# Performance work log

Hardware: AMD Instinct MI355X
Metric: run time of the kernel (lower is better)

## Reference

```python
import jax, jax.numpy as jnp
import numpy as np
import math

N, D, H, E = 4096, 128, 8, 131072
HD = D // H  # head_dim = 16
SCALE = 1.0 / math.sqrt(HD)


def ln(x, g, b, eps=1e-5):
    m = x.mean(-1, keepdims=True)
    v = ((x - m) ** 2).mean(-1, keepdims=True)
    return (x - m) * jax.lax.rsqrt(v + eps) * g + b


def setup_inputs() -> dict:
    key = jax.random.key(0)
    ks = iter(jax.random.split(key, 40))

    def lin(out_d, in_d):
        w = jax.random.normal(next(ks), (out_d, in_d), jnp.float32) / math.sqrt(in_d)
        b = jnp.zeros((out_d,), jnp.float32)
        return w, b

    x = jax.random.normal(next(ks), (N, D), jnp.float32)
    edge_index = jax.random.randint(next(ks), (2, E), 0, N, dtype=jnp.int64)
    wq_l, bq_l = lin(D, D); wk_l, bk_l = lin(D, D); wv_l, bv_l = lin(D, D)
    wg, bg = lin(D, 2 * D)
    wq_g, bq_g = lin(D, D); wk_g, bk_g = lin(D, D); wv_g, bv_g = lin(D, D)
    wo_g, bo_g = lin(D, D)
    wf, bf = lin(D, 2 * D)
    gf = jnp.ones((D,), jnp.float32); betaf = jnp.zeros((D,), jnp.float32)
    w1, b1 = lin(4 * D, D); w2, b2 = lin(D, 4 * D)
    g1 = jnp.ones((D,), jnp.float32); be1 = jnp.zeros((D,), jnp.float32)
    g2 = jnp.ones((D,), jnp.float32); be2 = jnp.zeros((D,), jnp.float32)
    return dict(x=x, edge_index=edge_index,
                wq_l=wq_l, bq_l=bq_l, wk_l=wk_l, bk_l=bk_l, wv_l=wv_l, bv_l=bv_l,
                wg=wg, bg=bg,
                wq_g=wq_g, bq_g=bq_g, wk_g=wk_g, bk_g=bk_g, wv_g=wv_g, bv_g=bv_g,
                wo_g=wo_g, bo_g=bo_g,
                wf=wf, bf=bf, gf=gf, betaf=betaf,
                w1=w1, b1=b1, w2=w2, b2=b2,
                g1=g1, be1=be1, g2=g2, be2=be2)


def reference(x, edge_index, wq_l, bq_l, wk_l, bk_l, wv_l, bv_l, wg, bg,
              wq_g, bq_g, wk_g, bk_g, wv_g, bv_g, wo_g, bo_g,
              wf, bf, gf, betaf, w1, b1, w2, b2, g1, be1, g2, be2):
    src, dst = edge_index[0], edge_index[1]  # PyG: j=source, i=target
    # ---- local edge-indexed multi-head attention (GraphInteractionModule) ----
    Q = (x @ wq_l.T + bq_l).reshape(N, H, HD)
    K = (x @ wk_l.T + bk_l).reshape(N, H, HD)
    V = (x @ wv_l.T + bv_l).reshape(N, H, HD)
    attn = (Q[dst] * K[src]).sum(-1) * SCALE            # [E, H]
    m = jax.ops.segment_max(attn, dst, num_segments=N)  # [N, H]
    e = jnp.exp(attn - m[dst])
    s = jax.ops.segment_sum(e, dst, num_segments=N)
    alpha = e / s[dst]                                  # segment softmax over edges into each dst
    agg = jax.ops.segment_sum(V[src] * alpha[..., None], dst, num_segments=N).reshape(N, D)
    gate = jax.nn.sigmoid(jnp.concatenate([x, agg], axis=-1) @ wg.T + bg)
    local = gate * agg + (1.0 - gate) * x
    # ---- global dense MHA over all nodes (B=1) ----
    xn = ln(x, g1, be1)
    q = (xn @ wq_g.T + bq_g).reshape(N, H, HD)
    k = (xn @ wk_g.T + bk_g).reshape(N, H, HD)
    v = (xn @ wv_g.T + bv_g).reshape(N, H, HD)
    scores = jnp.einsum('nhd,mhd->hnm', q, k) * SCALE   # [H, N, N]
    p = jax.nn.softmax(scores, axis=-1)
    go = jnp.einsum('hnm,mhd->nhd', p, v).reshape(N, D) @ wo_g.T + bo_g
    # ---- fusion + residual + FFN ----
    fused = jax.nn.relu(ln(jnp.concatenate([local, go], axis=-1) @ wf.T + bf, gf, betaf))
    h = x + fused
    h2 = ln(h, g2, be2)
    out = h + (jax.nn.gelu(h2 @ w1.T + b1, approximate=False) @ w2.T + b2)
    return out
```

## Files before the change

kernel.cpp:

```cpp
#include <hip/hip_runtime.h>
#include <math.h>

#define NN 4096
#define DM 128
#define NE 131072
#define QSCALE 0.36067376022224085f
#define ESCALE 0.36067376022224085f

typedef short short8 __attribute__((ext_vector_type(8)));
typedef float f32x4  __attribute__((ext_vector_type(4)));
typedef unsigned int uint4v __attribute__((ext_vector_type(4)));

static __device__ __forceinline__ unsigned pk2(float lo, float hi) {
  union { float f; unsigned u; } a, b; a.f = lo; b.f = hi;
  return __builtin_amdgcn_perm(b.u + 0x8000u, a.u + 0x8000u, 0x07060302u);
}
static __device__ __forceinline__ unsigned pkp(float lo, float hi) {
  union { float f; unsigned u; } a, b; a.f = lo; b.f = hi;
  return __builtin_amdgcn_perm(b.u, a.u, 0x07060302u);
}
static __device__ __forceinline__ unsigned short f2bh(float f) {
  union { float f; unsigned u; } v; v.f = f;
  return (unsigned short)((v.u + 0x8000u) >> 16);
}
// ... 70 lines not shown
  }
  const int g = blockIdx.y >> 1;
  const float* Wt  = (g==0)?W0:(g==1)?W1:(g==2)?W2:(g==3)?W3:(g==4)?W4:W5;
  const float* Bia = (g==0)?B0:(g==1)?B1:(g==2)?B2:(g==3)?B3:(g==4)?B4:B5;
  void* Cp         = (g==0)?O0:(g==1)?O1:(g==2)?O2:(g==3)?O3:(g==4)?O4:O5;
  const int omode  = (g==4)?3:(g==5)?2:1;
  const float osc  = (g==3)? QSCALE : (g==0)? ESCALE : 1.f;
  const int m0 = blockIdx.x * 64, n0 = (blockIdx.y & 1) * 64;
  const int tid = threadIdx.x;
  const int srow = tid >> 2, koff = (tid & 3) * 8;
  const int lane = tid & 63, wave = tid >> 6;
  const int quad = lane >> 4, m16 = lane & 15;

  const float* arow = X + (size_t)(m0 + srow) * 128 + koff;
  float4 a0[4], a1[4];
#pragma unroll
  for (int c = 0; c < 4; c++) {
    a0[c] = *(const float4*)(arow + c * 32);
    a1[c] = *(const float4*)(arow + c * 32 + 4);
  }
  if (g >= 3) {
    float s = 0.f;
#pragma unroll
    for (int c = 0; c < 4; c++)
      s += a0[c].x + a0[c].y + a0[c].z + a0[c].w + a1[c].x + a1[c].y + a1[c].z + a1[c].w;
    s += __shfl_xor(s, 1); s += __shfl_xor(s, 2);
    float mean = s * (1.0f / 128.0f);
    float v = 0.f;
#pragma unroll
    for (int c = 0; c < 4; c++) {
      float d;
      d = a0[c].x - mean; v += d*d;  d = a0[c].y - mean; v += d*d;
      d = a0[c].z - mean; v += d*d;  d = a0[c].w - mean; v += d*d;
      d = a1[c].x - mean; v += d*d;  d = a1[c].y - mean; v += d*d;
      d = a1[c].z - mean; v += d*d;  d = a1[c].w - mean; v += d*d;
    }
    v += __shfl_xor(v, 1); v += __shfl_xor(v, 2);
    float rstd = rsqrtf(v * (1.0f / 128.0f) + 1e-5f);
#pragma unroll
    for (int c = 0; c < 4; c++) {
      const int col = c * 32 + koff;
      float4 gv0 = *(const float4*)(G1 + col),  gv1 = *(const float4*)(G1 + col + 4);
      float4 bv0 = *(const float4*)(Be1 + col), bv1 = *(const float4*)(Be1 + col + 4);
      LN1(a0[c].x, gv0.x, bv0.x); LN1(a0[c].y, gv0.y, bv0.y);
      LN1(a0[c].z, gv0.z, bv0.z); LN1(a0[c].w, gv0.w, bv0.w);
      LN1(a1[c].x, gv1.x, bv1.x); LN1(a1[c].y, gv1.y, bv1.y);
      LN1(a1[c].z, gv1.z, bv1.z); LN1(a1[c].w, gv1.w, bv1.w);
    }
  }

  f32x4 acc[4];
#pragma unroll
  for (int i = 0; i < 4; i++) acc[i] = {0.f, 0.f, 0.f, 0.f};
#pragma unroll
  for (int c = 0; c < 4; c++) {
    const float* wp = Wt + (size_t)(n0 + srow) * 128 + c * 32 + koff;
    float4 w0 = *(const float4*)wp, w1v = *(const float4*)(wp + 4);
    __syncthreads();
    *(short8*)&Asm[srow][koff] = cvt8(a0[c], a1[c]);
    *(short8*)&Wsm[srow][koff] = cvt8(w0, w1v);
    __syncthreads();
    short8 af = *(short8*)&Asm[wave * 16 + m16][quad * 8];
#pragma unroll
    for (int nt = 0; nt < 4; nt++) {
      short8 bf = *(short8*)&Wsm[nt * 16 + m16][quad * 8];
      acc[nt] = __builtin_amdgcn_mfma_f32_16x16x32_bf16(af, bf, acc[nt], 0, 0, 0);
    }
  }
#pragma unroll
  for (int nt = 0; nt < 4; nt++) {
#pragma unroll
    for (int r = 0; r < 4; r++) {
      const int m = m0 + wave * 16 + quad * 4 + r;
      const int n = n0 + nt * 16 + m16;
      float v = (acc[nt][r] + Bia[n]) * osc;
      size_t oi = (size_t)m * 128 + n;
      if (omode == 1)      ((unsigned short*)Cp)[oi] = f2bh(v);
      else if (omode == 3) ((unsigned short*)Cp)[(size_t)(n >> 4) * (NN * 16) + (size_t)m * 16 + (n & 15)] = f2bh(v);
      else                 ((unsigned short*)Cp)[(size_t)n * NN + m] = f2bh(v);
    }
  }
}

__global__ __launch_bounds__(256) void gemm_gate(
    const float* __restrict__ X, const float* __restrict__ AGG,
    const float* __restrict__ Wg, const float* __restrict__ Bg,
    float* __restrict__ LOCAL)
{
  __shared__ short Asm[64][40];
  __shared__ short Wsm[64][40];
  const int m0 = blockIdx.x * 64, n0 = blockIdx.y * 64;
  const int tid = threadIdx.x;
  const int srow = tid >> 2, koff = (tid & 3) * 8;
  const int lane = tid & 63, wave = tid >> 6;
  const int quad = lane >> 4, m16 = lane & 15;
  f32x4 acc[4];
#pragma unroll
  for (int i = 0; i < 4; i++) acc[i] = {0.f, 0.f, 0.f, 0.f};

  for (int k0 = 0; k0 < 256; k0 += 32) {
    const int kg = k0 + koff;
    const float* ap = (kg < 128) ? (X + (size_t)(m0 + srow) * 128 + kg)
                                 : (AGG + (size_t)(m0 + srow) * 128 + (kg - 128));
    float4 a0 = *(const float4*)ap, a1 = *(const float4*)(ap + 4);
    const float* wp = Wg + (size_t)(n0 + srow) * 256 + kg;
    float4 w0 = *(const float4*)wp, w1v = *(const float4*)(wp + 4);
    __syncthreads();
    *(short8*)&Asm[srow][koff] = cvt8(a0, a1);
    *(short8*)&Wsm[srow][koff] = cvt8(w0, w1v);
    __syncthreads();
    short8 af = *(short8*)&Asm[wave * 16 + m16][quad * 8];
#pragma unroll
    for (int nt = 0; nt < 4; nt++) {
      short8 bf = *(short8*)&Wsm[nt * 16 + m16][quad * 8];
      acc[nt] = __builtin_amdgcn_mfma_f32_16x16x32_bf16(af, bf, acc[nt], 0, 0, 0);
    }
  }
#pragma unroll
  for (int nt = 0; nt < 4; nt++) {
#pragma unroll
    for (int r = 0; r < 4; r++) {
      const int m = m0 + wave * 16 + quad * 4 + r;
      const int n = n0 + nt * 16 + m16;
      float v = acc[nt][r] + Bg[n];
      size_t oi = (size_t)m * 128 + n;
      float gg = 1.0f / (1.0f + __expf(fminf(fmaxf(-v, -80.f), 80.f)));
      LOCAL[oi] = gg * AGG[oi] + (1.0f - gg) * X[oi];
    }
  }
}

__global__ __launch_bounds__(256) void gemm_fuse(
    const float* __restrict__ LOCAL, const float* __restrict__ GO,
    const float* __restrict__ WF, const float* __restrict__ WC,
    const float* __restrict__ BF, const float* __restrict__ BFOLD,
    float* __restrict__ OUT)
{
  __shared__ short Asm[64][40];
  __shared__ short Wsm[64][40];
  const int m0 = blockIdx.x * 64, n0 = blockIdx.y * 64;
  const int tid = threadIdx.x;
  const int srow = tid >> 2, koff = (tid & 3) * 8;
  const int lane = tid & 63, wave = tid >> 6;
  const int quad = lane >> 4, m16 = lane & 15;
  f32x4 acc[4];
#pragma unroll
  for (int i = 0; i < 4; i++) acc[i] = {0.f, 0.f, 0.f, 0.f};

  for (int k0 = 0; k0 < 256; k0 += 32) {
    const int kg = k0 + koff;
    const float* ap = (kg < 128) ? (LOCAL + (size_t)(m0 + srow) * 128 + kg)
                                 : (GO + (size_t)(m0 + srow) * 128 + (kg - 128));
    float4 a0 = *(const float4*)ap, a1 = *(const float4*)(ap + 4);
    const float* wp = (kg < 128) ? (WF + (size_t)(n0 + srow) * 256 + kg)
                                 : (WC + (size_t)(n0 + srow) * 128 + (kg - 128));
    float4 w0 = *(const float4*)wp, w1v = *(const float4*)(wp + 4);
    __syncthreads();
    *(short8*)&Asm[srow][koff] = cvt8(a0, a1);
    *(short8*)&Wsm[srow][koff] = cvt8(w0, w1v);
    __syncthreads();
    short8 af = *(short8*)&Asm[wave * 16 + m16][quad * 8];
#pragma unroll
    for (int nt = 0; nt < 4; nt++) {
      short8 bf = *(short8*)&Wsm[nt * 16 + m16][quad * 8];
      acc[nt] = __builtin_amdgcn_mfma_f32_16x16x32_bf16(af, bf, acc[nt], 0, 0, 0);
    }
  }
#pragma unroll
  for (int nt = 0; nt < 4; nt++) {
#pragma unroll
    for (int r = 0; r < 4; r++) {
      const int m = m0 + wave * 16 + quad * 4 + r;
      const int n = n0 + nt * 16 + m16;
      size_t oi = (size_t)m * 128 + n;
      OUT[oi] = acc[nt][r] + BF[n] + BFOLD[n];
    }
  }
}

__global__ __launch_bounds__(512) void k_attn_fused(
    const unsigned short* __restrict__ Kh, const unsigned short* __restrict__ Qb,
    const unsigned short* __restrict__ VT, float* __restrict__ O,
    const int* __restrict__ EI, const unsigned short* __restrict__ Qb16,
    const unsigned short* __restrict__ Kb16,
    unsigned short* __restrict__ EB, int* __restrict__ deg)
{
  __shared__ float LO[8][4][16][16];
  __shared__ float LL[8][4][16];
  if (blockIdx.x >= 512) {
    int is64 = detect64(EI);
    int gid = (blockIdx.x - 512) * 512 + threadIdx.x;
    int e = gid >> 3, hh = gid & 7;
    int s = is64 ? EI[2*e]      : EI[e];
    int d = is64 ? EI[2*(NE+e)] : EI[NE+e];
    s = min(max(s, 0), NN-1); d = min(max(d, 0), NN-1);
    const uint4v* qp = (const uint4v*)(Qb16 + (size_t)d * DM + hh * 16);
    const uint4v* kp = (const uint4v*)(Kb16 + (size_t)s * DM + hh * 16);
    uint4v qa = qp[0], qb2 = qp[1];
    uint4v ka = kp[0], kb2 = kp[1];
    float acc = 0.f;
#pragma unroll
    for (int i2 = 0; i2 < 4; i2++) {
      acc += blo(qa[i2]) * blo(ka[i2]) + bhi(qa[i2]) * bhi(ka[i2]);
      acc += blo(qb2[i2]) * blo(kb2[i2]) + bhi(qb2[i2]) * bhi(kb2[i2]);
    }
    EB[(size_t)e*8 + hh] = f2bh(__builtin_amdgcn_exp2f(fminf(acc, 43.0f)));
    if (hh == 0) atomicAdd(&deg[d], 1);
    return;
  }
  const int h = blockIdx.x >> 6, qt = blockIdx.x & 63;
  const int tid = threadIdx.x, lane = tid & 63, wave = tid >> 6;
  const int quad = lane >> 4, m16 = lane & 15;
  const int r0 = qt * 64;
  const short8 z8 = {0,0,0,0,0,0,0,0};
  const f32x4  z4 = {0.f,0.f,0.f,0.f};
  short8 qf[4] = {z8, z8, z8, z8};
  if (quad < 2) {
#pragma unroll
    for (int j = 0; j < 4; j++)
      qf[j] = *(const short8*)(Qb + (size_t)(r0 + j * 16 + m16) * DM + h * 16 + quad * 8);
  }
  short8 ones;
#pragma unroll
  for (int i = 0; i < 8; i++) ones[i] = (short)0x3F80;
  const int kperm = (m16 >> 2) * 8 + (m16 & 3);
  const int kbase = wave * 512;
  const unsigned short* khead = Kh + (size_t)h * (NN * 16);
  f32x4 acc[4] = {z4, z4, z4, z4};
  f32x4 acc2[4] = {z4, z4, z4, z4};
  short8 a0 = z8, a1 = z8, a2 = z8, a3 = z8;
  for (int kt = 0; kt < 8; kt++) {
    const int key0 = kbase + kt * 64;
    if (quad < 2) {
      const unsigned short* kp = khead + (size_t)(key0 + kperm) * 16 + quad * 8;
      a0 = *(const short8*)kp;
      a1 = *(const short8*)(kp + 4 * 16);
      a2 = *(const short8*)(kp + 32 * 16);
      a3 = *(const short8*)(kp + 36 * 16);
    }
    const unsigned short* vp = VT + (size_t)(h * 16 + m16) * NN + key0 + quad * 8;
    short8 av0 = *(const short8*)vp;
    short8 av1 = *(const short8*)(vp + 32);
#pragma unroll
    for (int j = 0; j < 4; j++) {
      f32x4 s0 = __builtin_amdgcn_mfma_f32_16x16x32_bf16(a0, qf[j], z4, 0, 0, 0);
      f32x4 s1 = __builtin_amdgcn_mfma_f32_16x16x32_bf16(a1, qf[j], z4, 0, 0, 0);
      f32x4 s2 = __builtin_amdgcn_mfma_f32_16x16x32_bf16(a2, qf[j], z4, 0, 0, 0);
      f32x4 s3 = __builtin_amdgcn_mfma_f32_16x16x32_bf16(a3, qf[j], z4, 0, 0, 0);
      float e0 = __builtin_amdgcn_exp2f(s0[0]), e1 = __builtin_amdgcn_exp2f(s0[1]);
      float e2 = __builtin_amdgcn_exp2f(s0[2]), e3 = __builtin_amdgcn_exp2f(s0[3]);
      float e4 = __builtin_amdgcn_exp2f(s1[0]), e5 = __builtin_amdgcn_exp2f(s1[1]);
      float e6 = __builtin_amdgcn_exp2f(s1[2]), e7 = __builtin_amdgcn_exp2f(s1[3]);
      uint4v u;
      u.x = pkp(e0, e1); u.y = pkp(e2, e3); u.z = pkp(e4, e5); u.w = pkp(e6, e7);
      short8 p0 = __builtin_bit_cast(short8, u);
      float f0 = __builtin_amdgcn_exp2f(s2[0]), f1 = __builtin_amdgcn_exp2f(s2[1]);
      float f2 = __builtin_amdgcn_exp2f(s2[2]), f3 = __builtin_amdgcn_exp2f(s2[3]);
      float f4 = __builtin_amdgcn_exp2f(s3[0]), f5 = __builtin_amdgcn_exp2f(s3[1]);
      float f6 = __builtin_amdgcn_exp2f(s3[2]), f7 = __builtin_amdgcn_exp2f(s3[3]);
      uint4v w;
      w.x = pkp(f0, f1); w.y = pkp(f2, f3); w.z = pkp(f4, f5); w.w = pkp(f6, f7);
      short8 p1 = __builtin_bit_cast(short8, w);
      acc[j]  = __builtin_amdgcn_mfma_f32_16x16x32_bf16(av0, p0, acc[j], 0, 0, 0);
      acc[j]  = __builtin_amdgcn_mfma_f32_16x16x32_bf16(av1, p1, acc[j], 0, 0, 0);
      acc2[j] = __builtin_amdgcn_mfma_f32_16x16x32_bf16(ones, p0, acc2[j], 0, 0, 0);
      acc2[j] = __builtin_amdgcn_mfma_f32_16x16x32_bf16(ones, p1, acc2[j], 0, 0, 0);
    }
  }
#pragma unroll
  for (int j = 0; j < 4; j++) {
    float4 a4; a4.x = acc[j][0]; a4.y = acc[j][1]; a4.z = acc[j][2]; a4.w = acc[j][3];
    *(float4*)&LO[wave][j][m16][quad * 4] = a4;
    if (lane < 16) LL[wave][j][lane] = acc2[j][0];
  }
  __syncthreads();
  if (wave < 4) {
    const int j = wave;
    float4 o = *(float4*)&LO[0][j][m16][quad * 4];
    float lt = LL[0][j][m16];
#pragma unroll
    for (int w2 = 1; w2 < 8; w2++) {
      float4 t = *(float4*)&LO[w2][j][m16][quad * 4];
      o.x += t.x; o.y += t.y; o.z += t.z; o.w += t.w;
      lt += LL[w2][j][m16];
    }
    float inv = 1.0f / fmaxf(lt, 1e-30f);
    float4 r4; r4.x = o.x * inv; r4.y = o.y * inv; r4.z = o.z * inv; r4.w = o.w * inv;
    *(float4*)(O + (size_t)(r0 + j * 16 + m16) * DM + h * 16 + quad * 4) = r4;
  }
}

__global__ __launch_bounds__(256) void gemm_ffn1(
    const float* __restrict__ T, const float* __restrict__ X,
    const float* __restrict__ Gf, const float* __restrict__ Bef,
    const float* __restrict__ G2, const float* __restrict__ Be2,
    const float* __restrict__ W1, const float* __restrict__ B1,
    float* __restrict__ H, unsigned short* __restrict__ T1)
{
  __shared__ short Asm[64][40];
  __shared__ short Wsm[64][40];
  const int m0 = blockIdx.x * 64, n0 = blockIdx.y * 64;
  const int tid = threadIdx.x;
  const int srow = tid >> 2, koff = (tid & 3) * 8;
  const int lane = tid & 63, wave = tid >> 6;
  const int quad = lane >> 4, m16 = lane & 15;

  const float* trow = T + (size_t)(m0 + srow) * 128 + koff;
  const float* xrow = X + (size_t)(m0 + srow) * 128 + koff;
  float4 a0[4], a1[4];
#pragma unroll
  for (int c = 0; c < 4; c++) {
    a0[c] = *(const float4*)(trow + c * 32);
    a1[c] = *(const float4*)(trow + c * 32 + 4);
  }
  {
    float s = 0.f;
#pragma unroll
    for (int c = 0; c < 4; c++)
      s += a0[c].x + a0[c].y + a0[c].z + a0[c].w + a1[c].x + a1[c].y + a1[c].z + a1[c].w;
    s += __shfl_xor(s, 1); s += __shfl_xor(s, 2);
    float mean = s * (1.0f / 128.0f);
    float v = 0.f;
#pragma unroll
    for (int c = 0; c < 4; c++) {
      float d;
      d = a0[c].x - mean; v += d*d;  d = a0[c].y - mean; v += d*d;
      d = a0[c].z - mean; v += d*d;  d = a0[c].w - mean; v += d*d;
      d = a1[c].x - mean; v += d*d;  d = a1[c].y - mean; v += d*d;
      d = a1[c].z - mean; v += d*d;  d = a1[c].w - mean; v += d*d;
    }
    v += __shfl_xor(v, 1); v += __shfl_xor(v, 2);
    float rstd = rsqrtf(v * (1.0f / 128.0f) + 1e-5f);
#pragma unroll
    for (int c = 0; c < 4; c++) {
      const int col = c * 32 + koff;
      float4 gv0 = *(const float4*)(Gf + col),  gv1 = *(const float4*)(Gf + col + 4);
      float4 bv0 = *(const float4*)(Bef + col), bv1 = *(const float4*)(Bef + col + 4);
      float4 x0 = *(const float4*)(xrow + c * 32), x1 = *(const float4*)(xrow + c * 32 + 4);
      LN1(a0[c].x, gv0.x, bv0.x); LN1(a0[c].y, gv0.y, bv0.y);
      LN1(a0[c].z, gv0.z, bv0.z); LN1(a0[c].w, gv0.w, bv0.w);
      LN1(a1[c].x, gv1.x, bv1.x); LN1(a1[c].y, gv1.y, bv1.y);
      LN1(a1[c].z, gv1.z, bv1.z); LN1(a1[c].w, gv1.w, bv1.w);
      a0[c].x = x0.x + fmaxf(a0[c].x, 0.f); a0[c].y = x0.y + fmaxf(a0[c].y, 0.f);
      a0[c].z = x0.z + fmaxf(a0[c].z, 0.f); a0[c].w = x0.w + fmaxf(a0[c].w, 0.f);
      a1[c].x = x1.x + fmaxf(a1[c].x, 0.f); a1[c].y = x1.y + fmaxf(a1[c].y, 0.f);
      a1[c].z = x1.z + fmaxf(a1[c].z, 0.f); a1[c].w = x1.w + fmaxf(a1[c].w, 0.f);
      if (blockIdx.y == 0) {
        *(float4*)(H + (size_t)(m0 + srow) * 128 + c * 32 + koff)     = a0[c];
        *(float4*)(H + (size_t)(m0 + srow) * 128 + c * 32 + koff + 4) = a1[c];
      }
    }
  }
  {
    float s = 0.f;
#pragma unroll
    for (int c = 0; c < 4; c++)
      s += a0[c].x + a0[c].y + a0[c].z + a0[c].w + a1[c].x + a1[c].y + a1[c].z + a1[c].w;
    s += __shfl_xor(s, 1); s += __shfl_xor(s, 2);
    float mean = s * (1.0f / 128.0f);
    float v = 0.f;
#pragma unroll
    for (int c = 0; c < 4; c++) {
      float d;
      d = a0[c].x - mean; v += d*d;  d = a0[c].y - mean; v += d*d;
      d = a0[c].z - mean; v += d*d;  d = a0[c].w - mean; v += d*d;
      d = a1[c].x - mean; v += d*d;  d = a1[c].y - mean; v += d*d;
      d = a1[c].z - mean; v += d*d;  d = a1[c].w - mean; v += d*d;
    }
    v += __shfl_xor(v, 1); v += __shfl_xor(v, 2);
    float rstd = rsqrtf(v * (1.0f / 128.0f) + 1e-5f);
#pragma unroll
    for (int c = 0; c < 4; c++) {
      const int col = c * 32 + koff;
      float4 gv0 = *(const float4*)(G2 + col),  gv1 = *(const float4*)(G2 + col + 4);
      float4 bv0 = *(const float4*)(Be2 + col), bv1 = *(const float4*)(Be2 + col + 4);
      LN1(a0[c].x, gv0.x, bv0.x); LN1(a0[c].y, gv0.y, bv0.y);
      LN1(a0[c].z, gv0.z, bv0.z); LN1(a0[c].w, gv0.w, bv0.w);
      LN1(a1[c].x, gv1.x, bv1.x); LN1(a1[c].y, gv1.y, bv1.y);
      LN1(a1[c].z, gv1.z, bv1.z); LN1(a1[c].w, gv1.w, bv1.w);
    }
  }

  f32x4 acc[4];
#pragma unroll
  for (int i = 0; i < 4; i++) acc[i] = {0.f, 0.f, 0.f, 0.f};
#pragma unroll
  for (int c = 0; c < 4; c++) {
    const float* wp = W1 + (size_t)(n0 + srow) * 128 + c * 32 + koff;
    float4 w0 = *(const float4*)wp, w1v = *(const float4*)(wp + 4);
    __syncthreads();
    *(short8*)&Asm[srow][koff] = cvt8(a0[c], a1[c]);
    *(short8*)&Wsm[srow][koff] = cvt8(w0, w1v);
    __syncthreads();
    short8 af = *(short8*)&Asm[wave * 16 + m16][quad * 8];
#pragma unroll
    for (int nt = 0; nt < 4; nt++) {
      short8 bf = *(short8*)&Wsm[nt * 16 + m16][quad * 8];
      acc[nt] = __builtin_amdgcn_mfma_f32_16x16x32_bf16(af, bf, acc[nt], 0, 0, 0);
    }
  }
#pragma unroll
  for (int nt = 0; nt < 4; nt++) {
#pragma unroll
    for (int r = 0; r < 4; r++) {
      const int m = m0 + wave * 16 + quad * 4 + r;
      const int n = n0 + nt * 16 + m16;
      float v = acc[nt][r] + B1[n];
      v = 0.5f * v * (1.0f + erff(v * 0.70710678118654752f));
      T1[(size_t)m * 512 + n] = f2bh(v);
    }
  }
}

__global__ __launch_bounds__(256) void gemm_w2b(
    const unsigned short* __restrict__ A,
    const float* __restrict__ Wt, const float* __restrict__ Bias,
    const float* __restrict__ Res, float* __restrict__ Cp)
{
  __shared__ short Asm[64][40];
  __shared__ short Wsm[64][40];
  const int m0 = blockIdx.x * 64, n0 = blockIdx.y * 64;
  const int tid = threadIdx.x;
  const int srow = tid >> 2, koff = (tid & 3) * 8;
  const int lane = tid & 63, wave = tid >> 6;
  const int quad = lane >> 4, m16 = lane & 15;
  f32x4 acc[4];
#pragma unroll
  for (int i = 0; i < 4; i++) acc[i] = {0.f, 0.f, 0.f, 0.f};

  for (int k0 = 0; k0 < 512; k0 += 32) {
    const int kg = k0 + koff;
    short8 av = *(const short8*)(A + (size_t)(m0 + srow) * 512 + kg);
    const float* wp = Wt + (size_t)(n0 + srow) * 512 + kg;
    float4 w0 = *(const float4*)wp, w1v = *(const float4*)(wp + 4);
    __syncthreads();
    *(short8*)&Asm[srow][koff] = av;
    *(short8*)&Wsm[srow][koff] = cvt8(w0, w1v);
    __syncthreads();
    short8 af = *(short8*)&Asm[wave * 16 + m16][quad * 8];
#pragma unroll
    for (int nt = 0; nt < 4; nt++) {
      short8 bf = *(short8*)&Wsm[nt * 16 + m16][quad * 8];
      acc[nt] = __builtin_amdgcn_mfma_f32_16x16x32_bf16(af, bf, acc[nt], 0, 0, 0);
    }
  }
#pragma unroll
  for (int nt = 0; nt < 4; nt++) {
#pragma unroll
    for (int r = 0; r < 4; r++) {
      const int m = m0 + wave * 16 + quad * 4 + r;
      const int n = n0 + nt * 16 + m16;
      size_t oi = (size_t)m * 128 + n;
      Cp[oi] = acc[nt][r] + Bias[n] + Res[oi];
    }
  }
}

__global__ __launch_bounds__(256) void k_scan(const int* __restrict__ deg,
    int* __restrict__ offs, int* __restrict__ cursor) {
  __shared__ int sums[256];
  int t = threadIdx.x;
  int loc[16];
  int s = 0;
#pragma unroll
  for (int i = 0; i < 16; i++) { loc[i] = s; s += deg[t*16 + i]; }
  sums[t] = s;
  __syncthreads();
  for (int d = 1; d < 256; d <<= 1) {
    int v = (t >= d) ? sums[t - d] : 0;
    __syncthreads();
    sums[t] += v;
    __syncthreads();
  }
  int base = sums[t] - s;
#pragma unroll
  for (int i = 0; i < 16; i++) {
    offs[t*16 + i] = base + loc[i];
    cursor[t*16 + i] = base + loc[i];
  }
}
__global__ __launch_bounds__(256) void k_scatter(const int* __restrict__ EI,
    int* __restrict__ cursor, int* __restrict__ elist) {
  int is64 = detect64(EI);
  int e = blockIdx.x * 256 + threadIdx.x;
  int d = is64 ? EI[2*(NE+e)] : EI[NE+e];
  d = min(max(d, 0), NN-1);
  int slot = atomicAdd(&cursor[d], 1);
  elist[slot] = e;
}

__global__ __launch_bounds__(256) void k_edge_agg3(const int* __restrict__ EI,
    const int* __restrict__ deg, const int* __restrict__ offs,
    const int* __restrict__ elist, const unsigned short* __restrict__ Vl,
    const unsigned short* __restrict__ EB, float* __restrict__ AG) {
  __shared__ float PS[2][128];
  __shared__ float SSH[2][2][8];
  int is64 = detect64(EI);
  int tid = threadIdx.x;
  int dsti = tid >> 7;
  int half = (tid >> 6) & 1;
  int lane = tid & 63;
  int d = blockIdx.x * 2 + dsti;
  int degd = deg[d], start = offs[d];
  int hh = lane >> 3;
  float ss = 0.f;
  for (int i = (lane & 7) * 2 + half; i < degd; i += 16)
    ss += b2f16(EB[(size_t)elist[start + i] * 8 + hh]);
  for (int o = 1; o < 8; o <<= 1) ss += __shfl_xor(ss, o);
  if ((lane & 7) == 0) SSH[dsti][half][hh] = ss;
  __syncthreads();
  float inv = 1.0f / fmaxf(SSH[dsti][0][hh] + SSH[dsti][1][hh], 1e-30f);
  float ax = 0.f, ay = 0.f;
  int i = half;
  for (; i + 6 < degd; i += 8) {
    int e0 = elist[start+i], e1 = elist[start+i+2], e2 = elist[start+i+4], e3 = elist[start+i+6];
    int s0 = is64 ? EI[2*e0] : EI[e0];
    int s1 = is64 ? EI[2*e1] : EI[e1];
    int s2 = is64 ? EI[2*e2] : EI[e2];
    int s3 = is64 ? EI[2*e3] : EI[e3];
    s0 = min(max(s0,0),NN-1); s1 = min(max(s1,0),NN-1);
    s2 = min(max(s2,0),NN-1); s3 = min(max(s3,0),NN-1);
    float w0 = b2f16(EB[(size_t)e0*8 + hh]) * inv;
    float w1 = b2f16(EB[(size_t)e1*8 + hh]) * inv;
    float w2 = b2f16(EB[(size_t)e2*8 + hh]) * inv;
    float w3 = b2f16(EB[(size_t)e3*8 + hh]) * inv;
    unsigned v0 = *(const unsigned*)(Vl + (size_t)s0 * DM + 2 * lane);
    unsigned v1 = *(const unsigned*)(Vl + (size_t)s1 * DM + 2 * lane);
    unsigned v2 = *(const unsigned*)(Vl + (size_t)s2 * DM + 2 * lane);
    unsigned v3 = *(const unsigned*)(Vl + (size_t)s3 * DM + 2 * lane);
    ax += w0 * b2f16((unsigned short)(v0 & 0xffffu)) + w1 * b2f16((unsigned short)(v1 & 0xffffu))
        + w2 * b2f16((unsigned short)(v2 & 0xffffu)) + w3 * b2f16((unsigned short)(v3 & 0xffffu));
    ay += w0 * b2f16((unsigned short)(v0 >> 16)) + w1 * b2f16((unsigned short)(v1 >> 16))
        + w2 * b2f16((unsigned short)(v2 >> 16)) + w3 * b2f16((unsigned short)(v3 >> 16));
  }
  for (; i < degd; i += 2) {
    int e = elist[start + i];
    int s = is64 ? EI[2*e] : EI[e];
    s = min(max(s, 0), NN-1);
    float a = b2f16(EB[(size_t)e*8 + hh]) * inv;
    unsigned v = *(const unsigned*)(Vl + (size_t)s * DM + 2 * lane);
    ax += a * b2f16((unsigned short)(v & 0xffffu));
    ay += a * b2f16((unsigned short)(v >> 16));
  }
  if (half == 1) { PS[dsti][2*lane] = ax; PS[dsti][2*lane+1] = ay; }
  __syncthreads();
  if (half == 0) {
    float2 r; r.x = ax + PS[dsti][2*lane]; r.y = ay + PS[dsti][2*lane+1];
    *(float2*)(AG + (size_t)d * DM + 2 * lane) = r;
  }
}

extern "C" void kernel_launch(void* const* d_in, const int* in_sizes, int n_in,
                              void* d_out, int out_size, void* d_ws, size_t ws_size,
                              hipStream_t stream) {
  const float* x     = (const float*)d_in[0];
  const int*   ei    = (const int*)  d_in[1];
  const float* wq_l  = (const float*)d_in[2];  const float* bq_l = (const float*)d_in[3];
  const float* wk_l  = (const float*)d_in[4];  const float* bk_l = (const float*)d_in[5];
  const float* wv_l  = (const float*)d_in[6];  const float* bv_l = (const float*)d_in[7];
  const float* wg    = (const float*)d_in[8];  const float* bg   = (const float*)d_in[9];
  const float* wq_g  = (const float*)d_in[10]; const float* bq_g = (const float*)d_in[11];
  const float* wk_g  = (const float*)d_in[12]; const float* bk_g = (const float*)d_in[13];
  const float* wv_g  = (const float*)d_in[14]; const float* bv_g = (const float*)d_in[15];
  const float* wo_g  = (const float*)d_in[16]; const float* bo_g = (const float*)d_in[17];
  const float* wf    = (const float*)d_in[18]; const float* bff  = (const float*)d_in[19];
  const float* gf    = (const float*)d_in[20]; const float* betaf= (const float*)d_in[21];
  const float* w1    = (const float*)d_in[22]; const float* b1   = (const float*)d_in[23];
  const float* w2    = (const float*)d_in[24]; const float* b2   = (const float*)d_in[25];
  const float* g1    = (const float*)d_in[26]; const float* be1  = (const float*)d_in[27];
  const float* g2    = (const float*)d_in[28]; const float* be2  = (const float*)d_in[29];
  float* out = (float*)d_out;

  const size_t NEED = (size_t)3305600 * 4;
  if (ws_size < NEED) {
    k_fill<<<2048, 256, 0, stream>>>(out, 100.0f, NN*DM);
    return;
  }

  float* W = (float*)d_ws;
  unsigned short* lQb   = (unsigned short*)(W + 0);
  unsigned short* lKb   = (unsigned short*)(W + 524288);
  unsigned short* lV    = (unsigned short*)(W + 1048576);
  unsigned short* eb    = (unsigned short*)(W + 1310720);
  float*          go    = W + 1835008;
  unsigned short* qgb   = (unsigned short*)(W + 2359296);
  unsigned short* kgb   = (unsigned short*)(W + 2621440);
  unsigned short* vgT   = (unsigned short*)(W + 2883584);
  float*          agg   = W + 0;
  float*          local_= W + 524288;
  float*          tmpf  = W + 2097152;
  float*          h     = W + 2621440;
  unsigned short* t1    = (unsigned short*)(W + 0);
  int* deg    = (int*)(W + 3145728);
  int* cursor = (int*)(W + 3149824);
  int* offs   = (int*)(W + 3153920);
  int* elist  = (int*)(W + 3158016);
  float* Wc    = W + 3289088;
  float* bfold = W + 3305472;

  dim3 b256(256);

  gemm_six<<<dim3(64,13), b256, 0, stream>>>(x, g1, be1,
      wq_l, wk_l, wv_l, wq_g, wk_g, wv_g,
      bq_l, bk_l, bv_l, bq_g, bk_g, bv_g,
      lQb, lKb, lV, qgb, kgb, vgT, deg,
      wf, wo_g, bo_g, Wc, bfold);

  k_attn_fused<<<2560, dim3(512), 0, stream>>>(kgb, qgb, vgT, go, ei, lQb, lKb, eb, deg);

  k_scan<<<1, b256, 0, stream>>>(deg, offs, cursor);
  k_scatter<<<512, b256, 0, stream>>>(ei, cursor, elist);
  k_edge_agg3<<<2048, b256, 0, stream>>>(ei, deg, offs, elist, lV, eb, agg);

  gemm_gate<<<dim3(64,2), b256, 0, stream>>>(x, agg, wg, bg, local_);

  gemm_fuse<<<dim3(64,2), b256, 0, stream>>>(local_, go, wf, Wc, bff, bfold, tmpf);

  gemm_ffn1<<<dim3(64,8), b256, 0, stream>>>(tmpf, x, gf, betaf, g2, be2, w1, b1, h, t1);
  gemm_w2b<<<dim3(64,2), b256, 0, stream>>>(t1, w2, b2, h, out);
}
```

Before: 220.2 us.

## Fuse gate, fusion, FFN1 and FFN2 GEMMs into one per-row-tile tail kernel

Replaces the four tail kernels (gate GEMM, fusion GEMM, FFN1 with layer norms, FFN2) with a single k_tail kernel. Each 64-row block computes all 128 output columns through every stage. The gated local result and the normalized activations stay in shared memory as bf16 instead of going through global memory. This removes three launches and some intermediate global traffic. The cost is a grid of only 64 blocks, each running many serial load-sync-MFMA iterations, so most of the GPU sits idle during the tail and latency may dominate.

After: 247.3 us. +12.3%, slower.

```diff
diff --git a/kernel.cpp b/kernel.cpp
--- a/kernel.cpp
+++ b/kernel.cpp
@@ -176,102 +176,6 @@
   }
 }
 
-__global__ __launch_bounds__(256) void gemm_gate(
-    const float* __restrict__ X, const float* __restrict__ AGG,
-    const float* __restrict__ Wg, const float* __restrict__ Bg,
-    float* __restrict__ LOCAL)
-{
-  __shared__ short Asm[64][40];
-  __shared__ short Wsm[64][40];
-  const int m0 = blockIdx.x * 64, n0 = blockIdx.y * 64;
-  const int tid = threadIdx.x;
-  const int srow = tid >> 2, koff = (tid & 3) * 8;
-  const int lane = tid & 63, wave = tid >> 6;
-  const int quad = lane >> 4, m16 = lane & 15;
-  f32x4 acc[4];
-#pragma unroll
-  for (int i = 0; i < 4; i++) acc[i] = {0.f, 0.f, 0.f, 0.f};
-
-  for (int k0 = 0; k0 < 256; k0 += 32) {
-    const int kg = k0 + koff;
-    const float* ap = (kg < 128) ? (X + (size_t)(m0 + srow) * 128 + kg)
-                                 : (AGG + (size_t)(m0 + srow) * 128 + (kg - 128));
-    float4 a0 = *(const float4*)ap, a1 = *(const float4*)(ap + 4);
-    const float* wp = Wg + (size_t)(n0 + srow) * 256 + kg;
-    float4 w0 = *(const float4*)wp, w1v = *(const float4*)(wp + 4);
-    __syncthreads();
-    *(short8*)&Asm[srow][koff] = cvt8(a0, a1);
-    *(short8*)&Wsm[srow][koff] = cvt8(w0, w1v);
-    __syncthreads();
-    short8 af = *(short8*)&Asm[wave * 16 + m16][quad * 8];
-#pragma unroll
-    for (int nt = 0; nt < 4; nt++) {
-      short8 bf = *(short8*)&Wsm[nt * 16 + m16][quad * 8];
-      acc[nt] = __builtin_amdgcn_mfma_f32_16x16x32_bf16(af, bf, acc[nt], 0, 0, 0);
-    }
-  }
-#pragma unroll
-  for (int nt = 0; nt < 4; nt++) {
-#pragma unroll
-    for (int r = 0; r < 4; r++) {
-      const int m = m0 + wave * 16 + quad * 4 + r;
-      const int n = n0 + nt * 16 + m16;
-      float v = acc[nt][r] + Bg[n];
-      size_t oi = (size_t)m * 128 + n;
-      float gg = 1.0f / (1.0f + __expf(fminf(fmaxf(-v, -80.f), 80.f)));
-      LOCAL[oi] = gg * AGG[oi] + (1.0f - gg) * X[oi];
-    }
-  }
-}
-
-__global__ __launch_bounds__(256) void gemm_fuse(
-    const float* __restrict__ LOCAL, const float* __restrict__ GO,
-    const float* __restrict__ WF, const float* __restrict__ WC,
-    const float* __restrict__ BF, const float* __restrict__ BFOLD,
-    float* __restrict__ OUT)
-{
-  __shared__ short Asm[64][40];
-  __shared__ short Wsm[64][40];
-  const int m0 = blockIdx.x * 64, n0 = blockIdx.y * 64;
-  const int tid = threadIdx.x;
-  const int srow = tid >> 2, koff = (tid & 3) * 8;
-  const int lane = tid & 63, wave = tid >> 6;
-  const int quad = lane >> 4, m16 = lane & 15;
-  f32x4 acc[4];
-#pragma unroll
-  for (int i = 0; i < 4; i++) acc[i] = {0.f, 0.f, 0.f, 0.f};
-
-  for (int k0 = 0; k0 < 256; k0 += 32) {
-    const int kg = k0 + koff;
-    const float* ap = (kg < 128) ? (LOCAL + (size_t)(m0 + srow) * 128 + kg)
-                                 : (GO + (size_t)(m0 + srow) * 128 + (kg - 128));
-    float4 a0 = *(const float4*)ap, a1 = *(const float4*)(ap + 4);
-    const float* wp = (kg < 128) ? (WF + (size_t)(n0 + srow) * 256 + kg)
-                                 : (WC + (size_t)(n0 + srow) * 128 + (kg - 128));
-    float4 w0 = *(const float4*)wp, w1v = *(const float4*)(wp + 4);
-    __syncthreads();
-    *(short8*)&Asm[srow][koff] = cvt8(a0, a1);
-    *(short8*)&Wsm[srow][koff] = cvt8(w0, w1v);
-    __syncthreads();
-    short8 af = *(short8*)&Asm[wave * 16 + m16][quad * 8];
-#pragma unroll
-    for (int nt = 0; nt < 4; nt++) {
-      short8 bf = *(short8*)&Wsm[nt * 16 + m16][quad * 8];
-      acc[nt] = __builtin_amdgcn_mfma_f32_16x16x32_bf16(af, bf, acc[nt], 0, 0, 0);
-    }
-  }
-#pragma unroll
-  for (int nt = 0; nt < 4; nt++) {
-#pragma unroll
-    for (int r = 0; r < 4; r++) {
-      const int m = m0 + wave * 16 + quad * 4 + r;
-      const int n = n0 + nt * 16 + m16;
-      size_t oi = (size_t)m * 128 + n;
-      OUT[oi] = acc[nt][r] + BF[n] + BFOLD[n];
-    }
-  }
-}
-
 __global__ __launch_bounds__(512) void k_attn_fused(
     const unsigned short* __restrict__ Kh, const unsigned short* __restrict__ Qb,
     const unsigned short* __restrict__ VT, float* __restrict__ O,
@@ -381,172 +285,6 @@
     float inv = 1.0f / fmaxf(lt, 1e-30f);
     float4 r4; r4.x = o.x * inv; r4.y = o.y * inv; r4.z = o.z * inv; r4.w = o.w * inv;
     *(float4*)(O + (size_t)(r0 + j * 16 + m16) * DM + h * 16 + quad * 4) = r4;
-  }
-}
-
-__global__ __launch_bounds__(256) void gemm_ffn1(
-    const float* __restrict__ T, const float* __restrict__ X,
-    const float* __restrict__ Gf, const float* __restrict__ Bef,
-    const float* __restrict__ G2, const float* __restrict__ Be2,
-    const float* __restrict__ W1, const float* __restrict__ B1,
-    float* __restrict__ H, unsigned short* __restrict__ T1)
-{
-  __shared__ short Asm[64][40];
-  __shared__ short Wsm[64][40];
-  const int m0 = blockIdx.x * 64, n0 = blockIdx.y * 64;
-  const int tid = threadIdx.x;
-  const int srow = tid >> 2, koff = (tid & 3) * 8;
-  const int lane = tid & 63, wave = tid >> 6;
-  const int quad = lane >> 4, m16 = lane & 15;
-
-  const float* trow = T + (size_t)(m0 + srow) * 128 + koff;
-  const float* xrow = X + (size_t)(m0 + srow) * 128 + koff;
-  float4 a0[4], a1[4];
-#pragma unroll
-  for (int c = 0; c < 4; c++) {
-    a0[c] = *(const float4*)(trow + c * 32);
-    a1[c] = *(const float4*)(trow + c * 32 + 4);
-  }
-  {
-    float s = 0.f;
-#pragma unroll
-    for (int c = 0; c < 4; c++)
-      s += a0[c].x + a0[c].y + a0[c].z + a0[c].w + a1[c].x + a1[c].y + a1[c].z + a1[c].w;
-    s += __shfl_xor(s, 1); s += __shfl_xor(s, 2);
-    float mean = s * (1.0f / 128.0f);
-    float v = 0.f;
-#pragma unroll
-    for (int c = 0; c < 4; c++) {
-      float d;
-      d = a0[c].x - mean; v += d*d;  d = a0[c].y - mean; v += d*d;
-      d = a0[c].z - mean; v += d*d;  d = a0[c].w - mean; v += d*d;
-      d = a1[c].x - mean; v += d*d;  d = a1[c].y - mean; v += d*d;
-      d = a1[c].z - mean; v += d*d;  d = a1[c].w - mean; v += d*d;
-    }
-    v += __shfl_xor(v, 1); v += __shfl_xor(v, 2);
-    float rstd = rsqrtf(v * (1.0f / 128.0f) + 1e-5f);
-#pragma unroll
-    for (int c = 0; c < 4; c++) {
-      const int col = c * 32 + koff;
-      float4 gv0 = *(const float4*)(Gf + col),  gv1 = *(const float4*)(Gf + col + 4);
-      float4 bv0 = *(const float4*)(Bef + col), bv1 = *(const float4*)(Bef + col + 4);
-      float4 x0 = *(const float4*)(xrow + c * 32), x1 = *(const float4*)(xrow + c * 32 + 4);
-      LN1(a0[c].x, gv0.x, bv0.x); LN1(a0[c].y, gv0.y, bv0.y);
-      LN1(a0[c].z, gv0.z, bv0.z); LN1(a0[c].w, gv0.w, bv0.w);
-      LN1(a1[c].x, gv1.x, bv1.x); LN1(a1[c].y, gv1.y, bv1.y);
-      LN1(a1[c].z, gv1.z, bv1.z); LN1(a1[c].w, gv1.w, bv1.w);
-      a0[c].x = x0.x + fmaxf(a0[c].x, 0.f); a0[c].y = x0.y + fmaxf(a0[c].y, 0.f);
-      a0[c].z = x0.z + fmaxf(a0[c].z, 0.f); a0[c].w = x0.w + fmaxf(a0[c].w, 0.f);
-      a1[c].x = x1.x + fmaxf(a1[c].x, 0.f); a1[c].y = x1.y + fmaxf(a1[c].y, 0.f);
-      a1[c].z = x1.z + fmaxf(a1[c].z, 0.f); a1[c].w = x1.w + fmaxf(a1[c].w, 0.f);
-      if (blockIdx.y == 0) {
-        *(float4*)(H + (size_t)(m0 + srow) * 128 + c * 32 + koff)     = a0[c];
-        *(float4*)(H + (size_t)(m0 + srow) * 128 + c * 32 + koff + 4) = a1[c];
-      }
-    }
-  }
-  {
-    float s = 0.f;
-#pragma unroll
-    for (int c = 0; c < 4; c++)
-      s += a0[c].x + a0[c].y + a0[c].z + a0[c].w + a1[c].x + a1[c].y + a1[c].z + a1[c].w;
-    s += __shfl_xor(s, 1); s += __shfl_xor(s, 2);
-    float mean = s * (1.0f / 128.0f);
-    float v = 0.f;
-#pragma unroll
-    for (int c = 0; c < 4; c++) {
-      float d;
-      d = a0[c].x - mean; v += d*d;  d = a0[c].y - mean; v += d*d;
-      d = a0[c].z - mean; v += d*d;  d = a0[c].w - mean; v += d*d;
-      d = a1[c].x - mean; v += d*d;  d = a1[c].y - mean; v += d*d;
-      d = a1[c].z - mean; v += d*d;  d = a1[c].w - mean; v += d*d;
-    }
-    v += __shfl_xor(v, 1); v += __shfl_xor(v, 2);
-    float rstd = rsqrtf(v * (1.0f / 128.0f) + 1e-5f);
-#pragma unroll
-    for (int c = 0; c < 4; c++) {
-      const int col = c * 32 + koff;
-      float4 gv0 = *(const float4*)(G2 + col),  gv1 = *(const float4*)(G2 + col + 4);
-      float4 bv0 = *(const float4*)(Be2 + col), bv1 = *(const float4*)(Be2 + col + 4);
-      LN1(a0[c].x, gv0.x, bv0.x); LN1(a0[c].y, gv0.y, bv0.y);
-      LN1(a0[c].z, gv0.z, bv0.z); LN1(a0[c].w, gv0.w, bv0.w);
-      LN1(a1[c].x, gv1.x, bv1.x); LN1(a1[c].y, gv1.y, bv1.y);
-      LN1(a1[c].z, gv1.z, bv1.z); LN1(a1[c].w, gv1.w, bv1.w);
-    }
-  }
-
-  f32x4 acc[4];
-#pragma unroll
-  for (int i = 0; i < 4; i++) acc[i] = {0.f, 0.f, 0.f, 0.f};
-#pragma unroll
-  for (int c = 0; c < 4; c++) {
-    const float* wp = W1 + (size_t)(n0 + srow) * 128 + c * 32 + koff;
-    float4 w0 = *(const float4*)wp, w1v = *(const float4*)(wp + 4);
-    __syncthreads();
-    *(short8*)&Asm[srow][koff] = cvt8(a0[c], a1[c]);
-    *(short8*)&Wsm[srow][koff] = cvt8(w0, w1v);
-    __syncthreads();
-    short8 af = *(short8*)&Asm[wave * 16 + m16][quad * 8];
-#pragma unroll
-    for (int nt = 0; nt < 4; nt++) {
-      short8 bf = *(short8*)&Wsm[nt * 16 + m16][quad * 8];
-      acc[nt] = __builtin_amdgcn_mfma_f32_16x16x32_bf16(af, bf, acc[nt], 0, 0, 0);
-    }
-  }
-#pragma unroll
-  for (int nt = 0; nt < 4; nt++) {
-#pragma unroll
-    for (int r = 0; r < 4; r++) {
-      const int m = m0 + wave * 16 + quad * 4 + r;
-      const int n = n0 + nt * 16 + m16;
-      float v = acc[nt][r] + B1[n];
-      v = 0.5f * v * (1.0f + erff(v * 0.70710678118654752f));
-      T1[(size_t)m * 512 + n] = f2bh(v);
-    }
-  }
-}
-
-__global__ __launch_bounds__(256) void gemm_w2b(
-    const unsigned short* __restrict__ A,
-    const float* __restrict__ Wt, const float* __restrict__ Bias,
-    const float* __restrict__ Res, float* __restrict__ Cp)
-{
-  __shared__ short Asm[64][40];
-  __shared__ short Wsm[64][40];
-  const int m0 = blockIdx.x * 64, n0 = blockIdx.y * 64;
-  const int tid = threadIdx.x;
-  const int srow = tid >> 2, koff = (tid & 3) * 8;
-  const int lane = tid & 63, wave = tid >> 6;
-  const int quad = lane >> 4, m16 = lane & 15;
-  f32x4 acc[4];
-#pragma unroll
-  for (int i = 0; i < 4; i++) acc[i] = {0.f, 0.f, 0.f, 0.f};
-
-  for (int k0 = 0; k0 < 512; k0 += 32) {
-    const int kg = k0 + koff;
-    short8 av = *(const short8*)(A + (size_t)(m0 + srow) * 512 + kg);
-    const float* wp = Wt + (size_t)(n0 + srow) * 512 + kg;
-    float4 w0 = *(const float4*)wp, w1v = *(const float4*)(wp + 4);
-    __syncthreads();
-    *(short8*)&Asm[srow][koff] = av;
-    *(short8*)&Wsm[srow][koff] = cvt8(w0, w1v);
-    __syncthreads();
-    short8 af = *(short8*)&Asm[wave * 16 + m16][quad * 8];
-#pragma unroll
-    for (int nt = 0; nt < 4; nt++) {
-      short8 bf = *(short8*)&Wsm[nt * 16 + m16][quad * 8];
-      acc[nt] = __builtin_amdgcn_mfma_f32_16x16x32_bf16(af, bf, acc[nt], 0, 0, 0);
-    }
-  }
-#pragma unroll
-  for (int nt = 0; nt < 4; nt++) {
-#pragma unroll
-    for (int r = 0; r < 4; r++) {
-      const int m = m0 + wave * 16 + quad * 4 + r;
-      const int n = n0 + nt * 16 + m16;
-      size_t oi = (size_t)m * 128 + n;
-      Cp[oi] = acc[nt][r] + Bias[n] + Res[oi];
-    }
   }
 }
 
@@ -644,6 +382,257 @@
   }
 }
 
+__global__ __launch_bounds__(256) void k_tail(
+    const float* __restrict__ X, const float* __restrict__ AGG, const float* __restrict__ GO,
+    const float* __restrict__ Wg, const float* __restrict__ Bg,
+    const float* __restrict__ WF, const float* __restrict__ WC,
+    const float* __restrict__ BF, const float* __restrict__ BFOLD,
+    const float* __restrict__ Gf, const float* __restrict__ Bef,
+    const float* __restrict__ G2, const float* __restrict__ Be2,
+    const float* __restrict__ W1, const float* __restrict__ B1,
+    const float* __restrict__ W2, const float* __restrict__ B2,
+    float* __restrict__ TMPF, float* __restrict__ H,
+    unsigned short* __restrict__ T1A, unsigned short* __restrict__ T1B,
+    float* __restrict__ OUT)
+{
+  __shared__ short Asm[64][40];
+  __shared__ short Wsm[128][40];
+  __shared__ short Lsm[4][64][40];
+  const int b = blockIdx.x;
+  const int m0 = b * 64;
+  const int tid = threadIdx.x;
+  const int srow = tid >> 2, koff = (tid & 3) * 8;
+  const int wrow = tid >> 1, koff2 = (tid & 1) * 16;
+  const int lane = tid & 63, wave = tid >> 6;
+  const int quad = lane >> 4, m16 = lane & 15;
+
+  unsigned short* t1a = T1A + (size_t)b * 16384;
+  unsigned short* t1b = T1B + (size_t)b * 16384;
+
+  f32x4 acc[8];
+
+#pragma unroll
+  for (int i = 0; i < 8; i++) acc[i] = {0.f, 0.f, 0.f, 0.f};
+  for (int k0 = 0; k0 < 256; k0 += 32) {
+    const int kg = k0 + koff;
+    const float* ap = (kg < 128) ? (X + (size_t)(m0 + srow) * 128 + kg)
+                                 : (AGG + (size_t)(m0 + srow) * 128 + (kg - 128));
+    float4 a0 = *(const float4*)ap, a1 = *(const float4*)(ap + 4);
+    const float* wp = Wg + (size_t)wrow * 256 + k0 + koff2;
+    float4 w0 = *(const float4*)wp,       w1v = *(const float4*)(wp + 4);
+    float4 w2v = *(const float4*)(wp + 8), w3v = *(const float4*)(wp + 12);
+    __syncthreads();
+    *(short8*)&Asm[srow][koff] = cvt8(a0, a1);
+    *(short8*)&Wsm[wrow][koff2]     = cvt8(w0, w1v);
+    *(short8*)&Wsm[wrow][koff2 + 8] = cvt8(w2v, w3v);
+    __syncthreads();
+    short8 af = *(short8*)&Asm[wave * 16 + m16][quad * 8];
+#pragma unroll
+    for (int nt = 0; nt < 8; nt++) {
+      short8 bf = *(short8*)&Wsm[nt * 16 + m16][quad * 8];
+      acc[nt] = __builtin_amdgcn_mfma_f32_16x16x32_bf16(af, bf, acc[nt], 0, 0, 0);
+    }
+  }
+  __syncthreads();
+#pragma unroll
+  for (int nt = 0; nt < 8; nt++) {
+#pragma unroll
+    for (int r = 0; r < 4; r++) {
+      const int mr = wave * 16 + quad * 4 + r;
+      const int n = nt * 16 + m16;
+      float v = acc[nt][r] + Bg[n];
+      size_t oi = (size_t)(m0 + mr) * 128 + n;
+      float gg = 1.0f / (1.0f + __expf(fminf(fmaxf(-v, -80.f), 80.f)));
+      float loc = gg * AGG[oi] + (1.0f - gg) * X[oi];
+      Lsm[n >> 5][mr][n & 31] = (short)f2bh(loc);
+    }
+  }
+
+#pragma unroll
+  for (int i = 0; i < 8; i++) acc[i] = {0.f, 0.f, 0.f, 0.f};
+  for (int k0 = 0; k0 < 256; k0 += 32) {
+    const int c = k0 >> 5;
+    float4 a0, a1;
+    if (c >= 4) {
+      const float* ap = GO + (size_t)(m0 + srow) * 128 + (k0 - 128) + koff;
+      a0 = *(const float4*)ap; a1 = *(const float4*)(ap + 4);
+    }
+    const float* wp = (k0 < 128) ? (WF + (size_t)wrow * 256 + k0 + koff2)
+                                 : (WC + (size_t)wrow * 128 + (k0 - 128) + koff2);
+    float4 w0 = *(const float4*)wp,       w1v = *(const float4*)(wp + 4);
+    float4 w2v = *(const float4*)(wp + 8), w3v = *(const float4*)(wp + 12);
+    __syncthreads();
+    if (c >= 4) *(short8*)&Asm[srow][koff] = cvt8(a0, a1);
+    *(short8*)&Wsm[wrow][koff2]     = cvt8(w0, w1v);
+    *(short8*)&Wsm[wrow][koff2 + 8] = cvt8(w2v, w3v);
+    __syncthreads();
+    short8 af = (c < 4) ? *(short8*)&Lsm[c][wave * 16 + m16][quad * 8]
+                        : *(short8*)&Asm[wave * 16 + m16][quad * 8];
+#pragma unroll
+    for (int nt = 0; nt < 8; nt++) {
+      short8 bf = *(short8*)&Wsm[nt * 16 + m16][quad * 8];
+      acc[nt] = __builtin_amdgcn_mfma_f32_16x16x32_bf16(af, bf, acc[nt], 0, 0, 0);
+    }
+  }
+#pragma unroll
+  for (int nt = 0; nt < 8; nt++) {
+#pragma unroll
+    for (int r = 0; r < 4; r++) {
+      const int mr = wave * 16 + quad * 4 + r;
+      const int n = nt * 16 + m16;
+      TMPF[(size_t)(m0 + mr) * 128 + n] = acc[nt][r] + BF[n] + BFOLD[n];
+    }
+  }
+  __syncthreads();
+
+  {
+    const float* trow = TMPF + (size_t)(m0 + srow) * 128 + koff;
+    const float* xrow = X + (size_t)(m0 + srow) * 128 + koff;
+    float4 a0[4], a1[4];
+#pragma unroll
+    for (int c = 0; c < 4; c++) {
+      a0[c] = *(const float4*)(trow + c * 32);
+      a1[c] = *(const float4*)(trow + c * 32 + 4);
+    }
+    {
+      float s = 0.f;
+#pragma unroll
+      for (int c = 0; c < 4; c++)
+        s += a0[c].x + a0[c].y + a0[c].z + a0[c].w + a1[c].x + a1[c].y + a1[c].z + a1[c].w;
+      s += __shfl_xor(s, 1); s += __shfl_xor(s, 2);
+      float mean = s * (1.0f / 128.0f);
+      float v = 0.f;
+#pragma unroll
+      for (int c = 0; c < 4; c++) {
+        float d;
+        d = a0[c].x - mean; v += d*d;  d = a0[c].y - mean; v += d*d;
+        d = a0[c].z - mean; v += d*d;  d = a0[c].w - mean; v += d*d;
+        d = a1[c].x - mean; v += d*d;  d = a1[c].y - mean; v += d*d;
+        d = a1[c].z - mean; v += d*d;  d = a1[c].w - mean; v += d*d;
+      }
+      v += __shfl_xor(v, 1); v += __shfl_xor(v, 2);
+      float rstd = rsqrtf(v * (1.0f / 128.0f) + 1e-5f);
+#pragma unroll
+      for (int c = 0; c < 4; c++) {
+        const int col = c * 32 + koff;
+        float4 gv0 = *(const float4*)(Gf + col),  gv1 = *(const float4*)(Gf + col + 4);
+        float4 bv0 = *(const float4*)(Bef + col), bv1 = *(const float4*)(Bef + col + 4);
+        float4 x0 = *(const float4*)(xrow + c * 32), x1 = *(const float4*)(xrow + c * 32 + 4);
+        LN1(a0[c].x, gv0.x, bv0.x); LN1(a0[c].y, gv0.y, bv0.y);
+        LN1(a0[c].z, gv0.z, bv0.z); LN1(a0[c].w, gv0.w, bv0.w);
+        LN1(a1[c].x, gv1.x, bv1.x); LN1(a1[c].y, gv1.y, bv1.y);
+        LN1(a1[c].z, gv1.z, bv1.z); LN1(a1[c].w, gv1.w, bv1.w);
+        a0[c].x = x0.x + fmaxf(a0[c].x, 0.f); a0[c].y = x0.y + fmaxf(a0[c].y, 0.f);
+        a0[c].z = x0.z + fmaxf(a0[c].z, 0.f); a0[c].w = x0.w + fmaxf(a0[c].w, 0.f);
+        a1[c].x = x1.x + fmaxf(a1[c].x, 0.f); a1[c].y = x1.y + fmaxf(a1[c].y, 0.f);
+        a1[c].z = x1.z + fmaxf(a1[c].z, 0.f); a1[c].w = x1.w + fmaxf(a1[c].w, 0.f);
+        *(float4*)(H + (size_t)(m0 + srow) * 128 + c * 32 + koff)     = a0[c];
+        *(float4*)(H + (size_t)(m0 + srow) * 128 + c * 32 + koff + 4) = a1[c];
+      }
+    }
+    {
+      float s = 0.f;
+#pragma unroll
+      for (int c = 0; c < 4; c++)
+        s += a0[c].x + a0[c].y + a0[c].z + a0[c].w + a1[c].x + a1[c].y + a1[c].z + a1[c].w;
+      s += __shfl_xor(s, 1); s += __shfl_xor(s, 2);
+      float mean = s * (1.0f / 128.0f);
+      float v = 0.f;
+#pragma unroll
+      for (int c = 0; c < 4; c++) {
+        float d;
+        d = a0[c].x - mean; v += d*d;  d = a0[c].y - mean; v += d*d;
+        d = a0[c].z - mean; v += d*d;  d = a0[c].w - mean; v += d*d;
+        d = a1[c].x - mean; v += d*d;  d = a1[c].y - mean; v += d*d;
+        d = a1[c].z - mean; v += d*d;  d = a1[c].w - mean; v += d*d;
+      }
+      v += __shfl_xor(v, 1); v += __shfl_xor(v, 2);
+      float rstd = rsqrtf(v * (1.0f / 128.0f) + 1e-5f);
+#pragma unroll
+      for (int c = 0; c < 4; c++) {
+        const int col = c * 32 + koff;
+        float4 gv0 = *(const float4*)(G2 + col),  gv1 = *(const float4*)(G2 + col + 4);
+        float4 bv0 = *(const float4*)(Be2 + col), bv1 = *(const float4*)(Be2 + col + 4);
+        LN1(a0[c].x, gv0.x, bv0.x); LN1(a0[c].y, gv0.y, bv0.y);
+        LN1(a0[c].z, gv0.z, bv0.z); LN1(a0[c].w, gv0.w, bv0.w);
+        LN1(a1[c].x, gv1.x, bv1.x); LN1(a1[c].y, gv1.y, bv1.y);
+        LN1(a1[c].z, gv1.z, bv1.z); LN1(a1[c].w, gv1.w, bv1.w);
+      }
+    }
+#pragma unroll
+    for (int c = 0; c < 4; c++)
+      *(short8*)&Lsm[c][srow][koff] = cvt8(a0[c], a1[c]);
+
+    for (int p = 0; p < 4; p++) {
+#pragma unroll
+      for (int i = 0; i < 8; i++) acc[i] = {0.f, 0.f, 0.f, 0.f};
+      for (int c = 0; c < 4; c++) {
+        const float* wp = W1 + (size_t)(p * 128 + wrow) * 128 + c * 32 + koff2;
+        float4 w0 = *(const float4*)wp,       w1v = *(const float4*)(wp + 4);
+        float4 w2v = *(const float4*)(wp + 8), w3v = *(const float4*)(wp + 12);
+        __syncthreads();
+        *(short8*)&Wsm[wrow][koff2]     = cvt8(w0, w1v);
+        *(short8*)&Wsm[wrow][koff2 + 8] = cvt8(w2v, w3v);
+        __syncthreads();
+        short8 af = *(short8*)&Lsm[c][wave * 16 + m16][quad * 8];
+#pragma unroll
+        for (int nt = 0; nt < 8; nt++) {
+          short8 bf = *(short8*)&Wsm[nt * 16 + m16][quad * 8];
+          acc[nt] = __builtin_amdgcn_mfma_f32_16x16x32_bf16(af, bf, acc[nt], 0, 0, 0);
+        }
+      }
+#pragma unroll
+      for (int nt = 0; nt < 8; nt++) {
+#pragma unroll
+        for (int r = 0; r < 4; r++) {
+          const int mr = wave * 16 + quad * 4 + r;
+          const int n = p * 128 + nt * 16 + m16;
+          float v = acc[nt][r] + B1[n];
+          v = 0.5f * v * (1.0f + erff(v * 0.70710678118654752f));
+          unsigned short* t1r = (mr < 32) ? (t1a + (size_t)mr * 512)
+                                          : (t1b + (size_t)(mr - 32) * 512);
+          t1r[n] = f2bh(v);
+        }
+      }
+    }
+  }
+  __syncthreads();
+
+#pragma unroll
+  for (int i = 0; i < 8; i++) acc[i] = {0.f, 0.f, 0.f, 0.f};
+  {
+    const unsigned short* t1r = (srow < 32) ? (t1a + (size_t)srow * 512)
+                                            : (t1b + (size_t)(srow - 32) * 512);
+    for (int k0 = 0; k0 < 512; k0 += 32) {
+      short8 av = *(const short8*)(t1r + k0 + koff);
+      const float* wp = W2 + (size_t)wrow * 512 + k0 + koff2;
+      float4 w0 = *(const float4*)wp,       w1v = *(const float4*)(wp + 4);
+      float4 w2v = *(const float4*)(wp + 8), w3v = *(const float4*)(wp + 12);
+      __syncthreads();
+      *(short8*)&Asm[srow][koff] = av;
+      *(short8*)&Wsm[wrow][koff2]     = cvt8(w0, w1v);
+      *(short8*)&Wsm[wrow][koff2 + 8] = cvt8(w2v, w3v);
+      __syncthreads();
+      short8 af = *(short8*)&Asm[wave * 16 + m16][quad * 8];
+#pragma unroll
+      for (int nt = 0; nt < 8; nt++) {
+        short8 bf = *(short8*)&Wsm[nt * 16 + m16][quad * 8];
+        acc[nt] = __builtin_amdgcn_mfma_f32_16x16x32_bf16(af, bf, acc[nt], 0, 0, 0);
+      }
+    }
+  }
+#pragma unroll
+  for (int nt = 0; nt < 8; nt++) {
+#pragma unroll
+    for (int r = 0; r < 4; r++) {
+      const int mr = wave * 16 + quad * 4 + r;
+      const int n = nt * 16 + m16;
+      size_t oi = (size_t)(m0 + mr) * 128 + n;
+      OUT[oi] = acc[nt][r] + B2[n] + H[oi];
+    }
+  }
+}
+
 extern "C" void kernel_launch(void* const* d_in, const int* in_sizes, int n_in,
                               void* d_out, int out_size, void* d_ws, size_t ws_size,
                               hipStream_t stream) {
@@ -681,10 +670,10 @@
   unsigned short* kgb   = (unsigned short*)(W + 2621440);
   unsigned short* vgT   = (unsigned short*)(W + 2883584);
   float*          agg   = W + 0;
-  float*          local_= W + 524288;
-  float*          tmpf  = W + 2097152;
+  float*          tmpf  = W + 1310720;
   float*          h     = W + 2621440;
-  unsigned short* t1    = (unsigned short*)(W + 0);
+  unsigned short* t1A   = (unsigned short*)(W + 0);
+  unsigned short* t1B   = (unsigned short*)(W + 524288);
   int* deg    = (int*)(W + 3145728);
   int* cursor = (int*)(W + 3149824);
   int* offs   = (int*)(W + 3153920);
@@ -706,10 +695,7 @@
   k_scatter<<<512, b256, 0, stream>>>(ei, cursor, elist);
   k_edge_agg3<<<2048, b256, 0, stream>>>(ei, deg, offs, elist, lV, eb, agg);
 
-  gemm_gate<<<dim3(64,2), b256, 0, stream>>>(x, agg, wg, bg, local_);
-
-  gemm_fuse<<<dim3(64,2), b256, 0, stream>>>(local_, go, wf, Wc, bff, bfold, tmpf);
-
-  gemm_ffn1<<<dim3(64,8), b256, 0, stream>>>(tmpf, x, gf, betaf, g2, be2, w1, b1, h, t1);
-  gemm_w2b<<<dim3(64,2), b256, 0, stream>>>(t1, w2, b2, h, out);
-}
+  k_tail<<<64, b256, 0, stream>>>(x, agg, go, wg, bg, wf, Wc, bff, bfold,
+      gf, betaf, g2, be2, w1, b1, w2, b2,
+      tmpf, h, t1A, t1B, out);
+}
```
